# Optimization experiments

Measured on AMD Instinct MI355X. Metric: run time of the kernel, lower is better.

The kernel has to match this reference:

```python
import jax, jax.numpy as jnp
import numpy as np

B, IN, H = 8192, 512, 512


def _binarize(w):
    # sign() forward with straight-through gradient (ebnn Binarize)
    return w + jax.lax.stop_gradient(jnp.sign(w) - w)


def setup_inputs() -> dict:
    key = jax.random.key(0)
    ks = jax.random.split(key, 7)
    stdv = 1.0 / np.sqrt(H)
    return {
        "x": jax.random.normal(ks[0], (B, IN), jnp.float32),
        "hx": jax.random.normal(ks[1], (B, H), jnp.float32),
        "cx": jax.random.normal(ks[2], (B, H), jnp.float32),
        "W_ih": jax.random.uniform(ks[3], (4 * H, IN), jnp.float32, -stdv, stdv),
        "W_hh": jax.random.uniform(ks[4], (4 * H, H), jnp.float32, -stdv, stdv),
        "bias_ih": jax.random.uniform(ks[5], (4 * H,), jnp.float32, -stdv, stdv),
        "bias_hh": jax.random.uniform(ks[6], (4 * H,), jnp.float32, -stdv, stdv),
    }


def reference(x, hx, cx, W_ih, W_hh, bias_ih, bias_hh):
    # gates: [B, 4H] = x @ sign(W_ih)^T + b_ih + hx @ sign(W_hh)^T + b_hh
    gates = (jnp.einsum("bi,gi->bg", x, _binarize(W_ih)) + bias_ih
             + jnp.einsum("bh,gh->bg", hx, _binarize(W_hh)) + bias_hh)
    ingate, forgetgate, cellgate, outgate = jnp.split(gates, 4, axis=1)
    cy = jax.nn.sigmoid(forgetgate) * cx + jax.nn.sigmoid(ingate) * jnp.tanh(cellgate)
    hy = jax.nn.sigmoid(outgate) * jnp.tanh(cy)
    return (hy, cy)
```

## Files before the change

### kernel.cpp

```cpp
#include <hip/hip_runtime.h>
#include <hip/hip_bf16.h>
#include <stdint.h>


typedef __attribute__((ext_vector_type(4))) int int4x;
typedef __attribute__((ext_vector_type(4))) float float4x;

#define B_DIM 8192
#define H_DIM 512

__device__ __forceinline__ float bf2f(uint16_t u) {
  return __uint_as_float(((uint32_t)u) << 16);
}
__device__ __forceinline__ uint16_t f2bf(float f) {
  uint32_t u = __float_as_uint(f);
  return (uint16_t)((u + 0x7FFFu + ((u >> 16) & 1u)) >> 16);
}
__device__ __forceinline__ float sigm(float x) { return 1.0f / (1.0f + __expf(-x)); }
__device__ __forceinline__ float tanh_f(float x) { return 2.0f / (1.0f + __expf(-2.0f * x)) - 1.0f; }

__device__ __forceinline__ int detect_f32(const void* x) {
  const int l = threadIdx.x & 63;
  uint32_t wrd = ((const uint32_t*)x)[l];
  uint32_t e0 = (wrd >> 7) & 0xFFu, e1 = (wrd >> 23) & 0xFFu;
  return __ballot(e0 > 0x85u || e1 > 0x85u) != 0ull;
}

__device__ __forceinline__ void quant4(const float* v, uint32_t* hi4, uint32_t* lo4) {
  uint32_t h = 0, lo = 0;
#pragma unroll
  for (int j = 0; j < 4; ++j) {
    float c = fminf(fmaxf(v[j], -8.0f), 8.0f);
    int xf = __float2int_rn(c * 4096.0f);
    xf = xf > 32639 ? 32639 : xf;
    xf = xf < -32768 ? -32768 : xf;
    const int lb = (xf << 24) >> 24;
    const int hb = (xf - lb) >> 8;
    lo |= ((uint32_t)lb & 0xFFu) << (8 * j);
    h |= ((uint32_t)hb & 0xFFu) << (8 * j);
  }
  *hi4 = h;
  *lo4 = lo;
}

__device__ __forceinline__ void gload16(const void* g, void* l) {
  __builtin_amdgcn_global_load_lds(
      (const __attribute__((address_space(1))) unsigned int*)g,
      (__attribute__((address_space(3))) unsigned int*)l, 16, 0, 0);
}

__global__ __launch_bounds__(256) void prep_kernel(
    const void* __restrict__ x, const void* __restrict__ hx,
    const void* __restrict__ w_ih, const void* __restrict__ w_hh,
    int8_t* __restrict__ Xhi, int8_t* __restrict__ Xlo, int8_t* __restrict__ Bp) {
  __shared__ alignas(16) char lsc[33280];
  const int isF32 = detect_f32(x);
  const int t = threadIdx.x;
  const int w = t >> 6, l = t & 63;
  const int isX = blockIdx.x < 512;
  const int grp = isX ? blockIdx.x : (blockIdx.x - 512);

#pragma unroll
  for (int rr = 0; rr < 4; ++rr) {
    const int r = w * 4 + rr;
    long rowbase;
    if (isX) rowbase = (long)(grp * 16 + r) * 512;
    else     rowbase = (long)((grp & 3) * 512 + (grp >> 2) * 16 + r) * 512;
#pragma unroll
    for (int src = 0; src < 2; ++src) {
      const void* sp_ = isX ? (src ? hx : x) : (src ? w_hh : w_ih);
#pragma unroll
      for (int q = 0; q < 2; ++q) {
        const int k = src * 512 + q * 256 + l * 4;
        float v[4];
        if (isF32) {
          float4x f = *(const float4x*)((const float*)sp_ + rowbase + q * 256 + l * 4);
          v[0] = f[0]; v[1] = f[1]; v[2] = f[2]; v[3] = f[3];
        } else {
          const uint16_t* s = (const uint16_t*)sp_ + rowbase + q * 256 + l * 4;
#pragma unroll
          for (int j = 0; j < 4; ++j) v[j] = bf2f(s[j]);
        }
        if (isX) {
          uint32_t h4, lo4;
          quant4(v, &h4, &lo4);
          *(uint32_t*)(lsc + r * 1040 + k) = h4;
          *(uint32_t*)(lsc + 16640 + r * 1040 + k) = lo4;
        } else {
          uint32_t s4 = 0;
#pragma unroll
          for (int j = 0; j < 4; ++j) {
            const int sv = v[j] > 0.f ? 1 : (v[j] < 0.f ? -1 : 0);
            s4 |= ((uint32_t)sv & 0xFFu) << (8 * j);
          }
          *(uint32_t*)(lsc + r * 1040 + k) = s4;
        }
      }
    }
  }
  __syncthreads();
  const int kt = t >> 4, quad = (t >> 2) & 3, rb = (t & 3) * 4;
  const int loff = kt * 64 + quad * 16;
  if (isX) {
    int4x h[4], lo[4];
#pragma unroll
    for (int i = 0; i < 4; ++i) {
      h[i] = *(const int4x*)(lsc + (rb + i) * 1040 + loff);
      lo[i] = *(const int4x*)(lsc + 16640 + (rb + i) * 1040 + loff);
    }
    int4x* dh = (int4x*)(Xhi + (long)grp * 16384 + t * 64);
    int4x* dl = (int4x*)(Xlo + (long)grp * 16384 + t * 64);
#pragma unroll
    for (int i = 0; i < 4; ++i) { dh[i] = h[i]; dl[i] = lo[i]; }
  } else {
    int4x s[4];
#pragma unroll
    for (int i = 0; i < 4; ++i)
      s[i] = *(const int4x*)(lsc + (rb + i) * 1040 + loff);
    int4x* db = (int4x*)(Bp + (long)grp * 16384 + t * 64);
#pragma unroll
    for (int i = 0; i < 4; ++i) db[i] = s[i];
  }
}

__global__ __launch_bounds__(512) void blstm_gemm_kernel(
    const int8_t* __restrict__ Xhi, const int8_t* __restrict__ Xlo,
    const int8_t* __restrict__ Bp, const void* __restrict__ b_ih,
    const void* __restrict__ b_hh, const void* __restrict__ cx,
    const void* __restrict__ xdet, void* __restrict__ out) {
  __shared__ alignas(16) char lds[49152];
  const int tid = threadIdx.x;
  const int l = tid & 63, w = tid >> 6;
  const int lrow = l & 15, lq = l >> 4;
  const int wy = w >> 1, wx = w & 1;
  const int isF32 = detect_f32(xdet);
  const int bid = blockIdx.x;
  const int by = (bid & 7) * 8 + ((bid >> 3) & 7);
  const int bx = bid >> 6;

  const int8_t* csrc[3];
  int cdst[3];
#pragma unroll
  for (int i = 0; i < 3; ++i) {
    const int c = w * 3 + i;
    if (c < 8) {
      csrc[i] = Xhi + (((long)(by * 8 + c)) << 14) + l * 16;
      cdst[i] = c * 1024;
    } else if (c < 16) {
      csrc[i] = Xlo + (((long)(by * 8 + (c - 8))) << 14) + l * 16;
      cdst[i] = 8192 + (c - 8) * 1024;
    } else {
      csrc[i] = Bp + (((long)(bx * 8 + (c - 16))) << 14) + l * 16;
      cdst[i] = 16384 + (c - 16) * 1024;
    }
  }

  int4x acch[2][4], accl[2][4];
#pragma unroll
  for (int mt = 0; mt < 2; ++mt)
#pragma unroll
    for (int g = 0; g < 4; ++g) {
      acch[mt][g] = (int4x){0, 0, 0, 0};
      accl[mt][g] = (int4x){0, 0, 0, 0};
    }

#pragma unroll
  for (int i = 0; i < 3; ++i) gload16(csrc[i], lds + cdst[i]);
  asm volatile("s_waitcnt vmcnt(0)\n\ts_barrier" ::: "memory");

#pragma unroll
  for (int ks = 0; ks < 16; ++ks) {
    const int cb = (ks & 1) * 24576;
    const int nb = cb ^ 24576;
    if (ks < 15) {
#pragma unroll
      for (int i = 0; i < 3; ++i)
        gload16(csrc[i] + (long)(ks + 1) * 1024, lds + nb + cdst[i]);
    }
    int4x ah[2], al[2], b[4];
#pragma unroll
    for (int mt = 0; mt < 2; ++mt) {
      ah[mt] = *(const int4x*)(lds + cb + (wy * 2 + mt) * 1024 + l * 16);
      al[mt] = *(const int4x*)(lds + cb + 8192 + (wy * 2 + mt) * 1024 + l * 16);
    }
#pragma unroll
    for (int g = 0; g < 4; ++g)
      b[g] = *(const int4x*)(lds + cb + 16384 + (wx * 4 + g) * 1024 + l * 16);
    __builtin_amdgcn_s_setprio(1);
#pragma unroll
    for (int mt = 0; mt < 2; ++mt)
#pragma unroll
      for (int g = 0; g < 4; ++g) {
        acch[mt][g] = __builtin_amdgcn_mfma_i32_16x16x64_i8(ah[mt], b[g], acch[mt][g], 0, 0, 0);
        accl[mt][g] = __builtin_amdgcn_mfma_i32_16x16x64_i8(al[mt], b[g], accl[mt][g], 0, 0, 0);
      }
    __builtin_amdgcn_s_setprio(0);
    if (ks < 15)
      asm volatile("s_waitcnt vmcnt(0)\n\ts_waitcnt lgkmcnt(0)\n\ts_barrier" ::: "memory");
  }

  const long CYo = (long)B_DIM * H_DIM;
  const int c = bx * 32 + wx * 16 + lrow;
  float biasv[4];
#pragma unroll
  for (int g = 0; g < 4; ++g) {
    if (isF32)
      biasv[g] = ((const float*)b_ih)[g * 512 + c] + ((const float*)b_hh)[g * 512 + c];
    else
      biasv[g] = bf2f(((const uint16_t*)b_ih)[g * 512 + c]) + bf2f(((const uint16_t*)b_hh)[g * 512 + c]);
  }
  float* outF = (float*)out;
  uint16_t* outB = (uint16_t*)out;
#pragma unroll
  for (int mt = 0; mt < 2; ++mt) {
#pragma unroll
    for (int r = 0; r < 4; ++r) {
      const int row = by * 128 + wy * 32 + mt * 16 + lq * 4 + r;
      const long cidx = (long)row * H_DIM + c;
      float vg[4];
#pragma unroll
      for (int g = 0; g < 4; ++g)
        vg[g] = fmaf((float)acch[mt][g][r], 0.0625f,
                     fmaf((float)accl[mt][g][r], 2.44140625e-4f, biasv[g]));
      const float cxv = isF32 ? ((const float*)cx)[cidx] : bf2f(((const uint16_t*)cx)[cidx]);
      const float ig = sigm(vg[0]), fg = sigm(vg[1]), og = sigm(vg[3]);
      const float cg = tanh_f(vg[2]);
      const float cy = fg * cxv + ig * cg;
      const float hy = og * tanh_f(cy);
      if (isF32) {
        outF[cidx] = hy;
        outF[CYo + cidx] = cy;
      } else {
        outB[cidx] = f2bf(hy);
        outB[CYo + cidx] = f2bf(cy);
      }
    }
  }
}

extern "C" void kernel_launch(void* const* d_in, const int* in_sizes, int n_in,
                              void* d_out, int out_size, void* d_ws, size_t ws_size,
                              hipStream_t stream) {
  const void* x = d_in[0];
  const void* hx = d_in[1];
  const void* cx = d_in[2];
  const void* W_ih = d_in[3];
  const void* W_hh = d_in[4];
  const void* b_ih = d_in[5];
  const void* b_hh = d_in[6];
  char* ws = (char*)d_ws;
  int8_t* Xhi = (int8_t*)ws;
  int8_t* Xlo = (int8_t*)(ws + 8388608);
  int8_t* Bp = (int8_t*)(ws + 16777216);

  prep_kernel<<<640, 256, 0, stream>>>(x, hx, W_ih, W_hh, Xhi, Xlo, Bp);
  blstm_gemm_kernel<<<1024, 512, 0, stream>>>(Xhi, Xlo, Bp, b_ih, b_hh, cx, x, d_out);
}
```

Measured before the change: 156.8 us.

## Triple-buffer GEMM LDS pipeline and widen prep kernel loads to 8 elements

```diff
diff --git a/kernel.cpp b/kernel.cpp
--- a/kernel.cpp
+++ b/kernel.cpp
@@ -69,32 +69,39 @@
 #pragma unroll
     for (int src = 0; src < 2; ++src) {
       const void* sp_ = isX ? (src ? hx : x) : (src ? w_hh : w_ih);
-#pragma unroll
-      for (int q = 0; q < 2; ++q) {
-        const int k = src * 512 + q * 256 + l * 4;
-        float v[4];
-        if (isF32) {
-          float4x f = *(const float4x*)((const float*)sp_ + rowbase + q * 256 + l * 4);
-          v[0] = f[0]; v[1] = f[1]; v[2] = f[2]; v[3] = f[3];
-        } else {
-          const uint16_t* s = (const uint16_t*)sp_ + rowbase + q * 256 + l * 4;
-#pragma unroll
-          for (int j = 0; j < 4; ++j) v[j] = bf2f(s[j]);
+      const int k = src * 512 + l * 8;
+      float v[8];
+      if (isF32) {
+        const float* fp = (const float*)sp_ + rowbase + l * 8;
+        float4x f0 = *(const float4x*)fp;
+        float4x f1 = *(const float4x*)(fp + 4);
+#pragma unroll
+        for (int j = 0; j < 4; ++j) { v[j] = f0[j]; v[4 + j] = f1[j]; }
+      } else {
+        int4x raw = *(const int4x*)((const uint16_t*)sp_ + rowbase + l * 8);
+        const uint16_t* u = (const uint16_t*)&raw;
+#pragma unroll
+        for (int j = 0; j < 8; ++j) v[j] = bf2f(u[j]);
+      }
+      if (isX) {
+        uint32_t h0, lo0, h1, lo1;
+        quant4(v, &h0, &lo0);
+        quant4(v + 4, &h1, &lo1);
+        *(uint32_t*)(lsc + r * 1040 + k) = h0;
+        *(uint32_t*)(lsc + r * 1040 + k + 4) = h1;
+        *(uint32_t*)(lsc + 16640 + r * 1040 + k) = lo0;
+        *(uint32_t*)(lsc + 16640 + r * 1040 + k + 4) = lo1;
+      } else {
+        uint32_t s0 = 0, s1 = 0;
+#pragma unroll
+        for (int j = 0; j < 4; ++j) {
+          const int a = v[j] > 0.f ? 1 : (v[j] < 0.f ? -1 : 0);
+          const int b = v[4 + j] > 0.f ? 1 : (v[4 + j] < 0.f ? -1 : 0);
+          s0 |= ((uint32_t)a & 0xFFu) << (8 * j);
+          s1 |= ((uint32_t)b & 0xFFu) << (8 * j);
         }
-        if (isX) {
-          uint32_t h4, lo4;
-          quant4(v, &h4, &lo4);
-          *(uint32_t*)(lsc + r * 1040 + k) = h4;
-          *(uint32_t*)(lsc + 16640 + r * 1040 + k) = lo4;
-        } else {
-          uint32_t s4 = 0;
-#pragma unroll
-          for (int j = 0; j < 4; ++j) {
-            const int sv = v[j] > 0.f ? 1 : (v[j] < 0.f ? -1 : 0);
-            s4 |= ((uint32_t)sv & 0xFFu) << (8 * j);
-          }
-          *(uint32_t*)(lsc + r * 1040 + k) = s4;
-        }
+        *(uint32_t*)(lsc + r * 1040 + k) = s0;
+        *(uint32_t*)(lsc + r * 1040 + k + 4) = s1;
       }
     }
   }
@@ -128,7 +135,7 @@
     const int8_t* __restrict__ Bp, const void* __restrict__ b_ih,
     const void* __restrict__ b_hh, const void* __restrict__ cx,
     const void* __restrict__ xdet, void* __restrict__ out) {
-  __shared__ alignas(16) char lds[49152];
+  __shared__ alignas(16) char lds[73728];
   const int tid = threadIdx.x;
   const int l = tid & 63, w = tid >> 6;
   const int lrow = l & 15, lq = l >> 4;
@@ -166,16 +173,18 @@
 
 #pragma unroll
   for (int i = 0; i < 3; ++i) gload16(csrc[i], lds + cdst[i]);
-  asm volatile("s_waitcnt vmcnt(0)\n\ts_barrier" ::: "memory");
+#pragma unroll
+  for (int i = 0; i < 3; ++i) gload16(csrc[i] + 1024, lds + 24576 + cdst[i]);
+  asm volatile("s_waitcnt vmcnt(3)\n\ts_barrier" ::: "memory");
 
 #pragma unroll
   for (int ks = 0; ks < 16; ++ks) {
-    const int cb = (ks & 1) * 24576;
-    const int nb = cb ^ 24576;
-    if (ks < 15) {
+    const int cb = (ks % 3) * 24576;
+    if (ks < 14) {
+      const int nb = ((ks + 2) % 3) * 24576;
 #pragma unroll
       for (int i = 0; i < 3; ++i)
-        gload16(csrc[i] + (long)(ks + 1) * 1024, lds + nb + cdst[i]);
+        gload16(csrc[i] + (long)(ks + 2) * 1024, lds + nb + cdst[i]);
     }
     int4x ah[2], al[2], b[4];
 #pragma unroll
@@ -195,7 +204,9 @@
         accl[mt][g] = __builtin_amdgcn_mfma_i32_16x16x64_i8(al[mt], b[g], accl[mt][g], 0, 0, 0);
       }
     __builtin_amdgcn_s_setprio(0);
-    if (ks < 15)
+    if (ks < 14)
+      asm volatile("s_waitcnt vmcnt(3)\n\ts_waitcnt lgkmcnt(0)\n\ts_barrier" ::: "memory");
+    else if (ks == 14)
       asm volatile("s_waitcnt vmcnt(0)\n\ts_waitcnt lgkmcnt(0)\n\ts_barrier" ::: "memory");
   }
 
```

After: 154.0 us. No clear change (-1.8%).
